# Kernel optimization log

Measured on AMD Instinct MI355X. Metric: run time of the kernel, lower is better.

The kernel has to match this reference:

```python
import jax, jax.numpy as jnp
import numpy as np

N = 50000      # num_nodes
E = 400000     # num_edges
H = 64         # h_dim
R = 200        # num_rels
B = 8          # num_bases (block-diagonal decomposition)


def setup_inputs() -> dict:
    ks = jax.random.split(jax.random.key(0), 10)
    s = 1.0 / np.sqrt(H).astype(np.float32)
    return {
        "emb":     jax.random.normal(ks[0], (N, H), jnp.float32),
        "norm":    jax.random.uniform(ks[1], (E, 1), jnp.float32),
        "eps":     jax.random.normal(ks[2], (N, H), jnp.float32),
        "w1":      jax.random.normal(ks[3], (R, B * 8 * 8), jnp.float32) * s,
        "loop_w1": jax.random.normal(ks[4], (H, H), jnp.float32) * s,
        "b1":      jnp.zeros((H,), jnp.float32),
        "w2":      jax.random.normal(ks[5], (R, B * 8 * 16), jnp.float32) * s,
        "loop_w2": jax.random.normal(ks[6], (H, 2 * H), jnp.float32) * s,
        "b2":      jnp.zeros((2 * H,), jnp.float32),
        "h_ids":   jnp.arange(N, dtype=jnp.int32),
        "src":     jax.random.randint(ks[7], (E,), 0, N, jnp.int32),
        "dst":     jax.random.randint(ks[8], (E,), 0, N, jnp.int32),
        "rel":     jax.random.randint(ks[9], (E,), 0, R, jnp.int32),
    }


def bdd_conv(feat, src, dst, rel, norm, weight, loop_w, bias, out_feat):
    # RelGraphConv with 'bdd' regularizer: per-edge relation-indexed
    # block-diagonal weight gather, bmm message, norm scale, scatter-add,
    # then bias + self-loop.
    n_edges = src.shape[0]
    sub_in = feat.shape[1] // B
    sub_out = out_feat // B
    w = weight[rel].reshape(n_edges, B, sub_in, sub_out)   # gather per edge
    x = feat[src].reshape(n_edges, B, sub_in)
    msg = jnp.einsum('ebi,ebio->ebo', x, w).reshape(n_edges, out_feat) * norm
    agg = jax.ops.segment_sum(msg, dst, num_segments=feat.shape[0])
    return agg + bias + feat @ loop_w


def reference(emb, norm, eps, w1, loop_w1, b1, w2, loop_w2, b2,
              h_ids, src, dst, rel):
    feat = emb[h_ids]                                       # embedding lookup
    h1 = jax.nn.relu(bdd_conv(feat, src, dst, rel, norm, w1, loop_w1, b1, H))
    h2 = bdd_conv(h1, src, dst, rel, norm, w2, loop_w2, b2, 2 * H)
    m, raw_v = jnp.split(h2, 2, axis=-1)                    # gaussian_parameters
    v = jax.nn.softplus(raw_v) + 1e-8
    return m + jnp.sqrt(v) * eps                            # reparameterize
```

## Files before the change

### kernel.cpp

```cpp
#include <hip/hip_runtime.h>
#include <math.h>


typedef __attribute__((ext_vector_type(8))) short bf16x8;
typedef __attribute__((ext_vector_type(4))) float f32x4;
typedef __attribute__((ext_vector_type(2))) float v2f;
typedef __attribute__((ext_vector_type(2))) _Float16 h2;

__device__ __forceinline__ int bcasti(int v, int l) {
    return __builtin_amdgcn_readlane(v, l);
}
__device__ __forceinline__ float bcastf(float v, int l) {
    return __int_as_float(__builtin_amdgcn_readlane(__float_as_int(v), l));
}
__device__ __forceinline__ unsigned short f2bf(float f) {
    unsigned u = __float_as_uint(f);
    return (unsigned short)((u + 0x7FFFu + ((u >> 16) & 1u)) >> 16);
}
__device__ __forceinline__ unsigned short f2h(float f) {
    return __builtin_bit_cast(unsigned short, (_Float16)f);
}
__device__ __forceinline__ float bfs(unsigned short s) { return __uint_as_float((unsigned)s << 16); }
__device__ __forceinline__ h2 uh2(unsigned u) { return __builtin_bit_cast(h2, u); }

__global__ void hist(const int* __restrict__ dst, int* __restrict__ deg, int e) {
    int i = blockIdx.x * blockDim.x + threadIdx.x;
    if (i < e) atomicAdd(&deg[dst[i]], 1);
}

__global__ void scan_part(const int* __restrict__ deg, int* __restrict__ bsum, int n) {
    __shared__ int sm[256];
    int t = threadIdx.x, g = blockIdx.x * 256 + t;
    sm[t] = (g < n) ? deg[g] : 0;
    __syncthreads();
    for (int d = 128; d > 0; d >>= 1) {
        if (t < d) sm[t] += sm[t + d];
        __syncthreads();
    }
    if (t == 0) bsum[blockIdx.x] = sm[0];
}

__global__ void scan_bsum(int* __restrict__ bsum, int* __restrict__ off, int nb, int n) {
    __shared__ int sm[256];
    int t = threadIdx.x;
    int v = (t < nb) ? bsum[t] : 0;
    sm[t] = v;
    __syncthreads();
    for (int d = 1; d < 256; d <<= 1) {
        int u = (t >= d) ? sm[t - d] : 0;
        __syncthreads();
        sm[t] += u;
        __syncthreads();
    }
    if (t < nb) bsum[t] = sm[t] - v;
    if (t == 255) off[n] = sm[255];
}

__global__ void scan_write(const int* __restrict__ deg, const int* __restrict__ bsum,
                           int* __restrict__ off, int n) {
    __shared__ int sm[256];
    int t = threadIdx.x, g = blockIdx.x * 256 + t;
    int v = (g < n) ? deg[g] : 0;
    sm[t] = v;
    __syncthreads();
    for (int d = 1; d < 256; d <<= 1) {
        int u = (t >= d) ? sm[t - d] : 0;
        __syncthreads();
        sm[t] += u;
        __syncthreads();
    }
    if (g < n) off[g] = bsum[blockIdx.x] + sm[t] - v;
}

__global__ void scatter_pack(const int* __restrict__ src, const int* __restrict__ dst,
                             const int* __restrict__ rel, const float* __restrict__ norm,
                             const int* __restrict__ h_ids, const int* __restrict__ off,
                             int* __restrict__ fil, unsigned* __restrict__ packA,
                             unsigned* __restrict__ packB, float* __restrict__ norm_s, int e) {
    int i = blockIdx.x * blockDim.x + threadIdx.x;
    if (i >= e) return;
    int d = dst[i];
    int p = off[d] + atomicAdd(&fil[d], 1);
    unsigned rhi = (unsigned)rel[i] << 16;
    int s = src[i];
    packA[p] = (unsigned)h_ids[s] | rhi;
    packB[p] = (unsigned)s | rhi;
    norm_s[p] = norm[i];
}

__global__ void cvt_all(const float* __restrict__ w1, const float* __restrict__ w2,
                        const float* __restrict__ emb, unsigned short* __restrict__ w1h,
                        unsigned short* __restrict__ w2h, unsigned short* __restrict__ embh,
                        int n1, int n2, int ne) {
    int i = blockIdx.x * blockDim.x + threadIdx.x;
    if (i < n1) w1h[i] = f2h(w1[i]);
    else if (i < n1 + n2) w2h[i - n1] = f2h(w2[i - n1]);
    else if (i < n1 + n2 + ne) embh[i - n1 - n2] = f2bf(emb[i - n1 - n2]);
}

__global__ __launch_bounds__(256) void
gemm1_mfma(const unsigned short* __restrict__ embh, const int* __restrict__ h_ids,
           const float* __restrict__ lw1, const float* __restrict__ b1,
           unsigned short* __restrict__ h1bh, int n_nodes) {
    int w = threadIdx.x >> 6, l = threadIdx.x & 63;
    int lr = l & 15, lq = l >> 4;
    int rt = blockIdx.x;
    bf16x8 bfr[2];
    int coln = w * 16 + lr;
#pragma unroll
    for (int kb = 0; kb < 2; ++kb)
#pragma unroll
        for (int jj = 0; jj < 8; ++jj)
            bfr[kb][jj] = (short)f2bf(lw1[(kb * 32 + lq * 8 + jj) * 64 + coln]);
    int nrow = rt * 16 + lr;
    if (nrow >= n_nodes) nrow = n_nodes - 1;
    const unsigned short* arow = embh + (long)h_ids[nrow] * 64 + lq * 8;
    bf16x8 af0 = *(const bf16x8*)arow;
    bf16x8 af1 = *(const bf16x8*)(arow + 32);
    f32x4 acc = {0.f, 0.f, 0.f, 0.f};
    acc = __builtin_amdgcn_mfma_f32_16x16x32_bf16(af0, bfr[0], acc, 0, 0, 0);
    acc = __builtin_amdgcn_mfma_f32_16x16x32_bf16(af1, bfr[1], acc, 0, 0, 0);
    float bb = b1[coln];
#pragma unroll
    for (int r = 0; r < 4; ++r) {
        int row = rt * 16 + lq * 4 + r;
        if (row < n_nodes) h1bh[(long)row * 64 + coln] = f2bf(acc[r] + bb);
    }
}

__global__ __launch_bounds__(256) void
gemm2_mfma(const unsigned short* __restrict__ h1h, const float* __restrict__ lw2,
           const float* __restrict__ b2, unsigned short* __restrict__ h2bh, int n_nodes) {
    int w = threadIdx.x >> 6, l = threadIdx.x & 63;
    int lr = l & 15, lq = l >> 4;
    int rt = blockIdx.x;
    bf16x8 bfr[2][2];
    int col0 = (2 * w) * 16 + lr, col1 = (2 * w + 1) * 16 + lr;
#pragma unroll
    for (int kb = 0; kb < 2; ++kb)
#pragma unroll
        for (int jj = 0; jj < 8; ++jj) {
            int k = kb * 32 + lq * 8 + jj;
            bfr[0][kb][jj] = (short)f2bf(lw2[k * 128 + col0]);
            bfr[1][kb][jj] = (short)f2bf(lw2[k * 128 + col1]);
        }
    int nrow = rt * 16 + lr;
    if (nrow >= n_nodes) nrow = n_nodes - 1;
    bf16x8 af0 = *(const bf16x8*)(h1h + (long)nrow * 64 + lq * 8);
    bf16x8 af1 = *(const bf16x8*)(h1h + (long)nrow * 64 + 32 + lq * 8);
    f32x4 acc0 = {0.f, 0.f, 0.f, 0.f}, acc1 = {0.f, 0.f, 0.f, 0.f};
    acc0 = __builtin_amdgcn_mfma_f32_16x16x32_bf16(af0, bfr[0][0], acc0, 0, 0, 0);
    acc0 = __builtin_amdgcn_mfma_f32_16x16x32_bf16(af1, bfr[0][1], acc0, 0, 0, 0);
    acc1 = __builtin_amdgcn_mfma_f32_16x16x32_bf16(af0, bfr[1][0], acc1, 0, 0, 0);
    acc1 = __builtin_amdgcn_mfma_f32_16x16x32_bf16(af1, bfr[1][1], acc1, 0, 0, 0);
    float bb0 = b2[col0], bb1 = b2[col1];
#pragma unroll
    for (int r = 0; r < 4; ++r) {
        int row = rt * 16 + lq * 4 + r;
        if (row < n_nodes) {
            h2bh[(long)row * 128 + col0] = f2bf(acc0[r] + bb0);
            h2bh[(long)row * 128 + col1] = f2bf(acc1[r] + bb1);
        }
    }
}

__device__ __forceinline__ float reduce8(float a0, float a1, float a2, float a3,
                                         float a4, float a5, float a6, float a7, int i) {
    int p1 = i & 1, p2 = (i >> 1) & 1, p3 = (i >> 2) & 1;
    float ka, sb, u0, u1, u2, u3, w0, w1;
    ka = p1 ? a1 : a0; sb = p1 ? a0 : a1; u0 = ka + __shfl_xor(sb, 1, 64);
    ka = p1 ? a3 : a2; sb = p1 ? a2 : a3; u1 = ka + __shfl_xor(sb, 1, 64);
    ka = p1 ? a5 : a4; sb = p1 ? a4 : a5; u2 = ka + __shfl_xor(sb, 1, 64);
    ka = p1 ? a7 : a6; sb = p1 ? a6 : a7; u3 = ka + __shfl_xor(sb, 1, 64);
    ka = p2 ? u1 : u0; sb = p2 ? u0 : u1; w0 = ka + __shfl_xor(sb, 2, 64);
    ka = p2 ? u3 : u2; sb = p2 ? u2 : u3; w1 = ka + __shfl_xor(sb, 2, 64);
    ka = p3 ? w1 : w0; sb = p3 ? w0 : w1;
    return ka + __shfl_xor(sb, 4, 64);
}

__global__ __launch_bounds__(256) void
edge1(const unsigned short* __restrict__ embh, const unsigned short* __restrict__ w1h,
      const unsigned short* __restrict__ h1bh, const int* __restrict__ off,
      const unsigned* __restrict__ packA, const float* __restrict__ norm_s,
      unsigned short* __restrict__ h1h, int n_nodes) {
    __shared__ unsigned short xstage[4][8][64];
    int tid = threadIdx.x;
    int w = tid >> 6, j = tid & 63, i = j & 7;
    int cl = j >> 3, il = j & 7;
    int n = blockIdx.x * 4 + w;
    if (n >= n_nodes) return;
    unsigned short* xsw = &xstage[w][0][0];
    float base = bfs(h1bh[(long)n * 64 + j]);
    h2 acc[4];
#pragma unroll
    for (int q = 0; q < 4; ++q) acc[q] = (h2){(_Float16)0.f, (_Float16)0.f};
    int e0 = off[n], e1v = off[n + 1];
    const long woff = (long)j * 8;
    for (int win = e0; win < e1v; win += 64) {
        int wcnt = e1v - win; if (wcnt > 64) wcnt = 64;
        unsigned u = (j < wcnt) ? packA[win + j] : 0u;
        float nmv = (j < wcnt) ? norm_s[win + j] : 0.f;
        for (int b8 = 0; b8 < wcnt; b8 += 8) {
            int cnt = wcnt - b8; if (cnt > 8) cnt = 8;
            int uc = __builtin_amdgcn_ds_bpermute((b8 + cl) << 2, (int)u);
            if (cl < cnt)
                *(bf16x8*)(xsw + (cl << 6) + (il << 3)) =
                    *(const bf16x8*)(embh + (long)((unsigned)uc & 0xFFFFu) * 64 + (il << 3));
            asm volatile("s_waitcnt lgkmcnt(0)" ::: "memory");
#pragma unroll
            for (int c = 0; c < 8; ++c)
                if (c < cnt) {
                    float nm = bcastf(nmv, b8 + c);
                    int rr = bcasti((int)u, b8 + c) >> 16;
                    uint4 wd = *(const uint4*)(w1h + (long)rr * 512 + woff);
                    _Float16 xh = (_Float16)(bfs(xsw[(c << 6) + j]) * nm);
                    h2 xh2 = {xh, xh};
                    acc[0] += xh2 * uh2(wd.x);
                    acc[1] += xh2 * uh2(wd.y);
                    acc[2] += xh2 * uh2(wd.z);
                    acc[3] += xh2 * uh2(wd.w);
                }
        }
    }
    float agg = reduce8((float)acc[0].x, (float)acc[0].y, (float)acc[1].x, (float)acc[1].y,
                        (float)acc[2].x, (float)acc[2].y, (float)acc[3].x, (float)acc[3].y, i);
    h1h[(long)n * 64 + j] = f2bf(fmaxf(base + agg, 0.f));
}

__global__ __launch_bounds__(256) void
edge2(const unsigned short* __restrict__ h1h, const unsigned short* __restrict__ w2h,
      const unsigned short* __restrict__ h2bh, const float* __restrict__ eps,
      const int* __restrict__ off, const unsigned* __restrict__ packB,
      const float* __restrict__ norm_s, float* __restrict__ out, int n_nodes) {
    __shared__ unsigned short xstage[4][8][64];
    int tid = threadIdx.x;
    int w = tid >> 6, j = tid & 63;
    int i = j & 7, b = j >> 3;
    int o1 = b * 16 + i, o2 = o1 + 8;
    int cl = j >> 3, il = j & 7;
    int n = blockIdx.x * 4 + w;
    if (n >= n_nodes) return;
    unsigned short* xsw = &xstage[w][0][0];
    float base1 = bfs(h2bh[(long)n * 128 + o1]);
    float base2 = bfs(h2bh[(long)n * 128 + o2]);
    h2 acc[8];
#pragma unroll
    for (int q = 0; q < 8; ++q) acc[q] = (h2){(_Float16)0.f, (_Float16)0.f};
    int e0 = off[n], e1v = off[n + 1];
    const long woff = (long)j * 16;
    for (int win = e0; win < e1v; win += 64) {
        int wcnt = e1v - win; if (wcnt > 64) wcnt = 64;
        unsigned u = (j < wcnt) ? packB[win + j] : 0u;
        float nmv = (j < wcnt) ? norm_s[win + j] : 0.f;
        for (int b8 = 0; b8 < wcnt; b8 += 8) {
            int cnt = wcnt - b8; if (cnt > 8) cnt = 8;
            int uc = __builtin_amdgcn_ds_bpermute((b8 + cl) << 2, (int)u);
            if (cl < cnt)
                *(bf16x8*)(xsw + (cl << 6) + (il << 3)) =
                    *(const bf16x8*)(h1h + (long)((unsigned)uc & 0xFFFFu) * 64 + (il << 3));
            asm volatile("s_waitcnt lgkmcnt(0)" ::: "memory");
#pragma unroll
            for (int c = 0; c < 8; ++c)
                if (c < cnt) {
                    float nm = bcastf(nmv, b8 + c);
                    int rr = bcasti((int)u, b8 + c) >> 16;
                    const uint4* p = (const uint4*)(w2h + (long)rr * 1024 + woff);
                    uint4 wa = p[0], wb = p[1];
                    _Float16 xh = (_Float16)(bfs(xsw[(c << 6) + j]) * nm);
                    h2 xh2 = {xh, xh};
                    acc[0] += xh2 * uh2(wa.x);
                    acc[1] += xh2 * uh2(wa.y);
                    acc[2] += xh2 * uh2(wa.z);
                    acc[3] += xh2 * uh2(wa.w);
                    acc[4] += xh2 * uh2(wb.x);
                    acc[5] += xh2 * uh2(wb.y);
                    acc[6] += xh2 * uh2(wb.z);
                    acc[7] += xh2 * uh2(wb.w);
                }
        }
    }
    float r1 = reduce8((float)acc[0].x, (float)acc[0].y, (float)acc[1].x, (float)acc[1].y,
                       (float)acc[2].x, (float)acc[2].y, (float)acc[3].x, (float)acc[3].y, i);
    float r2 = reduce8((float)acc[4].x, (float)acc[4].y, (float)acc[5].x, (float)acc[5].y,
                       (float)acc[6].x, (float)acc[6].y, (float)acc[7].x, (float)acc[7].y, i);
    float v1 = r1 + base1;
    float v2 = r2 + base2;
    float p1 = __shfl_xor(v1, 32, 64);
    float p2 = __shfl_xor(v2, 32, 64);
    if (j < 32) {
        long basep = (long)n * 64;
        float sp1 = (p1 > 20.f) ? p1 : log1pf(expf(p1));
        float sp2 = (p2 > 20.f) ? p2 : log1pf(expf(p2));
        out[basep + o1] = fmaf(sqrtf(sp1 + 1e-8f), eps[basep + o1], v1);
        out[basep + o2] = fmaf(sqrtf(sp2 + 1e-8f), eps[basep + o2], v2);
    }
}

extern "C" void kernel_launch(void* const* d_in, const int* in_sizes, int n_in,
                              void* d_out, int out_size, void* d_ws, size_t ws_size,
                              hipStream_t stream) {
    const float* emb   = (const float*)d_in[0];
    const float* norm  = (const float*)d_in[1];
    const float* eps   = (const float*)d_in[2];
    const float* w1    = (const float*)d_in[3];
    const float* lw1   = (const float*)d_in[4];
    const float* b1    = (const float*)d_in[5];
    const float* w2    = (const float*)d_in[6];
    const float* lw2   = (const float*)d_in[7];
    const float* b2    = (const float*)d_in[8];
    const int*   h_ids = (const int*)d_in[9];
    const int*   src   = (const int*)d_in[10];
    const int*   dst   = (const int*)d_in[11];
    const int*   rel   = (const int*)d_in[12];
    float* out = (float*)d_out;

    int n_nodes = in_sizes[0] / 64;
    int n_edges = in_sizes[10];
    int nw1 = in_sizes[3];
    int nw2 = in_sizes[6];
    int ne  = in_sizes[0];

    char* ws = (char*)d_ws;
    unsigned short* h1bh = (unsigned short*)ws;       ws += (size_t)n_nodes * 64 * 2;
    unsigned short* h1h  = (unsigned short*)ws;       ws += (size_t)n_nodes * 64 * 2;
    unsigned short* h2bh = (unsigned short*)ws;       ws += (size_t)n_nodes * 128 * 2;
    unsigned short* embh = (unsigned short*)ws;       ws += (size_t)ne * 2;
    unsigned short* w1h  = (unsigned short*)ws;       ws += (size_t)nw1 * 2;
    unsigned short* w2h  = (unsigned short*)ws;       ws += (size_t)nw2 * 2;
    unsigned* pkA = (unsigned*)ws;                    ws += (size_t)n_edges * 4;
    unsigned* pkB = (unsigned*)ws;                    ws += (size_t)n_edges * 4;
    float* norm_s = (float*)ws;                       ws += (size_t)n_edges * 4;
    int*   deg    = (int*)ws;                         ws += (size_t)n_nodes * 4;
    int*   fil    = (int*)ws;                         ws += (size_t)n_nodes * 4;
    int*   off    = (int*)ws;                         ws += (size_t)(n_nodes + 1) * 4;
    int*   bsum   = (int*)ws;

    int blk = 256;
    int nb = (n_nodes + 255) / 256;
    int nt = (n_nodes + 15) / 16;
    int ng = (n_nodes + 3) / 4;
    hipMemsetAsync(deg, 0, (size_t)n_nodes * 8, stream);
    cvt_all<<<(nw1 + nw2 + ne + blk - 1) / blk, blk, 0, stream>>>(w1, w2, emb, w1h, w2h, embh, nw1, nw2, ne);
    hist<<<(n_edges + blk - 1) / blk, blk, 0, stream>>>(dst, deg, n_edges);
    scan_part<<<nb, 256, 0, stream>>>(deg, bsum, n_nodes);
    scan_bsum<<<1, 256, 0, stream>>>(bsum, off, nb, n_nodes);
    scan_write<<<nb, 256, 0, stream>>>(deg, bsum, off, n_nodes);
    scatter_pack<<<(n_edges + blk - 1) / blk, blk, 0, stream>>>(src, dst, rel, norm, h_ids, off, fil, pkA, pkB, norm_s, n_edges);
    gemm1_mfma<<<nt, blk, 0, stream>>>(embh, h_ids, lw1, b1, h1bh, n_nodes);
    edge1<<<ng, blk, 0, stream>>>(embh, w1h, h1bh, off, pkA, norm_s, h1h, n_nodes);
    gemm2_mfma<<<nt, blk, 0, stream>>>(h1h, lw2, b2, h2bh, n_nodes);
    edge2<<<ng, blk, 0, stream>>>(h1h, w2h, h2bh, eps, off, pkB, norm_s, out, n_nodes);
}
```

Measured before the change: 268.7 us.

## Sort edges by relation and compute messages with per-relation MFMA GEMMs

Adds a relation histogram and scan so edges are bucketed by relation. Each relation's block-diagonal weight is expanded into a dense bf16 64xN matrix and applied to the gathered source features with MFMA. The fp16 messages go to a per-edge buffer, and separate kernels sum them per destination node through a position map. This swaps the per-edge scalar block-diagonal math for tensor-core GEMMs, at the cost of writing and re-reading a large message buffer (E x 128 fp16) and doing 8x redundant FLOPs on the zero blocks. A fallback keeps the old path when the workspace is too small.

```diff
diff --git a/kernel.cpp b/kernel.cpp
--- a/kernel.cpp
+++ b/kernel.cpp
@@ -4,12 +4,9 @@
 
 typedef __attribute__((ext_vector_type(8))) short bf16x8;
 typedef __attribute__((ext_vector_type(4))) float f32x4;
-typedef __attribute__((ext_vector_type(2))) float v2f;
 typedef __attribute__((ext_vector_type(2))) _Float16 h2;
 
-__device__ __forceinline__ int bcasti(int v, int l) {
-    return __builtin_amdgcn_readlane(v, l);
-}
+__device__ __forceinline__ int bcasti(int v, int l) { return __builtin_amdgcn_readlane(v, l); }
 __device__ __forceinline__ float bcastf(float v, int l) {
     return __int_as_float(__builtin_amdgcn_readlane(__float_as_int(v), l));
 }
@@ -17,15 +14,20 @@
     unsigned u = __float_as_uint(f);
     return (unsigned short)((u + 0x7FFFu + ((u >> 16) & 1u)) >> 16);
 }
-__device__ __forceinline__ unsigned short f2h(float f) {
+__device__ __forceinline__ unsigned short f2h16(float f) {
     return __builtin_bit_cast(unsigned short, (_Float16)f);
 }
 __device__ __forceinline__ float bfs(unsigned short s) { return __uint_as_float((unsigned)s << 16); }
 __device__ __forceinline__ h2 uh2(unsigned u) { return __builtin_bit_cast(h2, u); }
 
-__global__ void hist(const int* __restrict__ dst, int* __restrict__ deg, int e) {
+
+__global__ void hist2(const int* __restrict__ dst, const int* __restrict__ rel,
+                      int* __restrict__ deg, int* __restrict__ degr, int e) {
     int i = blockIdx.x * blockDim.x + threadIdx.x;
-    if (i < e) atomicAdd(&deg[dst[i]], 1);
+    if (i < e) {
+        atomicAdd(&deg[dst[i]], 1);
+        atomicAdd(&degr[rel[i]], 1);
+    }
 }
 
 __global__ void scan_part(const int* __restrict__ deg, int* __restrict__ bsum, int n) {
@@ -71,6 +73,301 @@
     }
     if (g < n) off[g] = bsum[blockIdx.x] + sm[t] - v;
 }
+
+__global__ void scan_rel(const int* __restrict__ degr, int* __restrict__ offr, int R) {
+    __shared__ int sm[256];
+    int t = threadIdx.x;
+    int v = (t < R) ? degr[t] : 0;
+    sm[t] = v;
+    __syncthreads();
+    for (int d = 1; d < 256; d <<= 1) {
+        int u = (t >= d) ? sm[t - d] : 0;
+        __syncthreads();
+        sm[t] += u;
+        __syncthreads();
+    }
+    if (t < R) offr[t] = sm[t] - v;
+    if (t == 255) offr[R] = sm[255];
+}
+
+__global__ void scatter2(const int* __restrict__ src, const int* __restrict__ dst,
+                         const int* __restrict__ rel, const float* __restrict__ norm,
+                         const int* __restrict__ h_ids, const int* __restrict__ off,
+                         const int* __restrict__ offr, int* __restrict__ fil,
+                         int* __restrict__ filr, int* __restrict__ pos,
+                         int* __restrict__ xidA, int* __restrict__ xidB,
+                         float* __restrict__ nrm, int e) {
+    int i = blockIdx.x * blockDim.x + threadIdx.x;
+    if (i >= e) return;
+    int d = dst[i], r = rel[i], s = src[i];
+    int p = offr[r] + atomicAdd(&filr[r], 1);
+    int q = off[d] + atomicAdd(&fil[d], 1);
+    pos[q] = p;
+    xidA[p] = h_ids[s];
+    xidB[p] = s;
+    nrm[p] = norm[i];
+}
+
+
+__global__ void cvt_new(const float* __restrict__ w1, const float* __restrict__ w2,
+                        const float* __restrict__ emb, unsigned short* __restrict__ w1dT,
+                        unsigned short* __restrict__ w2dT, unsigned short* __restrict__ embh,
+                        int R, int ne) {
+    int i = blockIdx.x * blockDim.x + threadIdx.x;
+    int n1d = R * 4096, n2d = R * 8192;
+    if (i < n1d) {
+        int r = i >> 12, rem = i & 4095;
+        int c = rem >> 6, k = rem & 63;
+        int b = k >> 3;
+        float v = (b == (c >> 3)) ? w1[(size_t)r * 512 + b * 64 + (k & 7) * 8 + (c & 7)] : 0.f;
+        w1dT[i] = f2bf(v);
+    } else if (i < n1d + n2d) {
+        int ii = i - n1d;
+        int r = ii >> 13, rem = ii & 8191;
+        int c = rem >> 6, k = rem & 63;
+        int b = k >> 3;
+        float v = (b == (c >> 4)) ? w2[(size_t)r * 1024 + b * 128 + (k & 7) * 16 + (c & 15)] : 0.f;
+        w2dT[ii] = f2bf(v);
+    } else if (i < n1d + n2d + ne) {
+        int ii = i - n1d - n2d;
+        embh[ii] = f2bf(emb[ii]);
+    }
+}
+
+__global__ void cvt_old(const float* __restrict__ w1, const float* __restrict__ w2,
+                        const float* __restrict__ emb, unsigned short* __restrict__ w1h,
+                        unsigned short* __restrict__ w2h, unsigned short* __restrict__ embh,
+                        int n1, int n2, int ne) {
+    int i = blockIdx.x * blockDim.x + threadIdx.x;
+    if (i < n1) w1h[i] = f2h16(w1[i]);
+    else if (i < n1 + n2) w2h[i - n1] = f2h16(w2[i - n1]);
+    else if (i < n1 + n2 + ne) embh[i - n1 - n2] = f2bf(emb[i - n1 - n2]);
+}
+
+
+__global__ __launch_bounds__(256) void
+gemm1_mfma(const unsigned short* __restrict__ embh, const int* __restrict__ h_ids,
+           const float* __restrict__ lw1, const float* __restrict__ b1,
+           unsigned short* __restrict__ h1bh, int n_nodes) {
+    int w = threadIdx.x >> 6, l = threadIdx.x & 63;
+    int lr = l & 15, lq = l >> 4;
+    int rt = blockIdx.x;
+    bf16x8 bfr[2];
+    int coln = w * 16 + lr;
+#pragma unroll
+    for (int kb = 0; kb < 2; ++kb)
+#pragma unroll
+        for (int jj = 0; jj < 8; ++jj)
+            bfr[kb][jj] = (short)f2bf(lw1[(kb * 32 + lq * 8 + jj) * 64 + coln]);
+    int nrow = rt * 16 + lr;
+    if (nrow >= n_nodes) nrow = n_nodes - 1;
+    const unsigned short* arow = embh + (long)h_ids[nrow] * 64 + lq * 8;
+    bf16x8 af0 = *(const bf16x8*)arow;
+    bf16x8 af1 = *(const bf16x8*)(arow + 32);
+    f32x4 acc = {0.f, 0.f, 0.f, 0.f};
+    acc = __builtin_amdgcn_mfma_f32_16x16x32_bf16(af0, bfr[0], acc, 0, 0, 0);
+    acc = __builtin_amdgcn_mfma_f32_16x16x32_bf16(af1, bfr[1], acc, 0, 0, 0);
+    float bb = b1[coln];
+#pragma unroll
+    for (int r = 0; r < 4; ++r) {
+        int row = rt * 16 + lq * 4 + r;
+        if (row < n_nodes) h1bh[(long)row * 64 + coln] = f2bf(acc[r] + bb);
+    }
+}
+
+__global__ __launch_bounds__(256) void
+gemm2_mfma(const unsigned short* __restrict__ h1h, const float* __restrict__ lw2,
+           const float* __restrict__ b2, unsigned short* __restrict__ h2bh, int n_nodes) {
+    int w = threadIdx.x >> 6, l = threadIdx.x & 63;
+    int lr = l & 15, lq = l >> 4;
+    int rt = blockIdx.x;
+    bf16x8 bfr[2][2];
+    int col0 = (2 * w) * 16 + lr, col1 = (2 * w + 1) * 16 + lr;
+#pragma unroll
+    for (int kb = 0; kb < 2; ++kb)
+#pragma unroll
+        for (int jj = 0; jj < 8; ++jj) {
+            int k = kb * 32 + lq * 8 + jj;
+            bfr[0][kb][jj] = (short)f2bf(lw2[k * 128 + col0]);
+            bfr[1][kb][jj] = (short)f2bf(lw2[k * 128 + col1]);
+        }
+    int nrow = rt * 16 + lr;
+    if (nrow >= n_nodes) nrow = n_nodes - 1;
+    bf16x8 af0 = *(const bf16x8*)(h1h + (long)nrow * 64 + lq * 8);
+    bf16x8 af1 = *(const bf16x8*)(h1h + (long)nrow * 64 + 32 + lq * 8);
+    f32x4 acc0 = {0.f, 0.f, 0.f, 0.f}, acc1 = {0.f, 0.f, 0.f, 0.f};
+    acc0 = __builtin_amdgcn_mfma_f32_16x16x32_bf16(af0, bfr[0][0], acc0, 0, 0, 0);
+    acc0 = __builtin_amdgcn_mfma_f32_16x16x32_bf16(af1, bfr[0][1], acc0, 0, 0, 0);
+    acc1 = __builtin_amdgcn_mfma_f32_16x16x32_bf16(af0, bfr[1][0], acc1, 0, 0, 0);
+    acc1 = __builtin_amdgcn_mfma_f32_16x16x32_bf16(af1, bfr[1][1], acc1, 0, 0, 0);
+    float bb0 = b2[col0], bb1 = b2[col1];
+#pragma unroll
+    for (int r = 0; r < 4; ++r) {
+        int row = rt * 16 + lq * 4 + r;
+        if (row < n_nodes) {
+            h2bh[(long)row * 128 + col0] = f2bf(acc0[r] + bb0);
+            h2bh[(long)row * 128 + col1] = f2bf(acc1[r] + bb1);
+        }
+    }
+}
+
+
+__global__ __launch_bounds__(256) void
+gemm_rel1(const unsigned short* __restrict__ embh, const unsigned short* __restrict__ w1dT,
+          const int* __restrict__ xidA, const float* __restrict__ nrm,
+          const int* __restrict__ offr, _Float16* __restrict__ msg1, int S) {
+    int r = blockIdx.x / S, s = blockIdx.x % S;
+    int w = threadIdx.x >> 6, l = threadIdx.x & 63;
+    int lr = l & 15, lq = l >> 4;
+    int e0r = offr[r], e1r = offr[r + 1];
+    if (e0r >= e1r) return;
+    bf16x8 bfr[4][2];
+    const unsigned short* wb = w1dT + (size_t)r * 4096;
+#pragma unroll
+    for (int ct = 0; ct < 4; ++ct)
+#pragma unroll
+        for (int kb = 0; kb < 2; ++kb)
+            bfr[ct][kb] = *(const bf16x8*)(wb + (ct * 16 + lr) * 64 + kb * 32 + lq * 8);
+    for (int t = s * 4 + w;; t += S * 4) {
+        int t16 = e0r + t * 16;
+        if (t16 >= e1r) break;
+        int erow = t16 + lr;
+        int erc = erow < e1r ? erow : e1r - 1;
+        const unsigned short* arow = embh + (size_t)xidA[erc] * 64 + lq * 8;
+        bf16x8 af0 = *(const bf16x8*)arow;
+        bf16x8 af1 = *(const bf16x8*)(arow + 32);
+        f32x4 acc[4];
+#pragma unroll
+        for (int ct = 0; ct < 4; ++ct) {
+            acc[ct] = (f32x4){0.f, 0.f, 0.f, 0.f};
+            acc[ct] = __builtin_amdgcn_mfma_f32_16x16x32_bf16(af0, bfr[ct][0], acc[ct], 0, 0, 0);
+            acc[ct] = __builtin_amdgcn_mfma_f32_16x16x32_bf16(af1, bfr[ct][1], acc[ct], 0, 0, 0);
+        }
+#pragma unroll
+        for (int r4 = 0; r4 < 4; ++r4) {
+            int orow = t16 + lq * 4 + r4;
+            int orc = orow < e1r ? orow : e1r - 1;
+            float nm = nrm[orc];
+            if (orow < e1r) {
+#pragma unroll
+                for (int ct = 0; ct < 4; ++ct)
+                    msg1[(size_t)orow * 64 + ct * 16 + lr] = (_Float16)(acc[ct][r4] * nm);
+            }
+        }
+    }
+}
+
+__global__ __launch_bounds__(256) void
+gemm_rel2(const unsigned short* __restrict__ h1h, const unsigned short* __restrict__ w2dT,
+          const int* __restrict__ xidB, const float* __restrict__ nrm,
+          const int* __restrict__ offr, _Float16* __restrict__ msg2, int S) {
+    int r = blockIdx.x / S, s = blockIdx.x % S;
+    int w = threadIdx.x >> 6, l = threadIdx.x & 63;
+    int lr = l & 15, lq = l >> 4;
+    int e0r = offr[r], e1r = offr[r + 1];
+    if (e0r >= e1r) return;
+    bf16x8 bfr[8][2];
+    const unsigned short* wb = w2dT + (size_t)r * 8192;
+#pragma unroll
+    for (int ct = 0; ct < 8; ++ct)
+#pragma unroll
+        for (int kb = 0; kb < 2; ++kb)
+            bfr[ct][kb] = *(const bf16x8*)(wb + (ct * 16 + lr) * 64 + kb * 32 + lq * 8);
+    for (int t = s * 4 + w;; t += S * 4) {
+        int t16 = e0r + t * 16;
+        if (t16 >= e1r) break;
+        int erow = t16 + lr;
+        int erc = erow < e1r ? erow : e1r - 1;
+        const unsigned short* arow = h1h + (size_t)xidB[erc] * 64 + lq * 8;
+        bf16x8 af0 = *(const bf16x8*)arow;
+        bf16x8 af1 = *(const bf16x8*)(arow + 32);
+        f32x4 acc[8];
+#pragma unroll
+        for (int ct = 0; ct < 8; ++ct) {
+            acc[ct] = (f32x4){0.f, 0.f, 0.f, 0.f};
+            acc[ct] = __builtin_amdgcn_mfma_f32_16x16x32_bf16(af0, bfr[ct][0], acc[ct], 0, 0, 0);
+            acc[ct] = __builtin_amdgcn_mfma_f32_16x16x32_bf16(af1, bfr[ct][1], acc[ct], 0, 0, 0);
+        }
+#pragma unroll
+        for (int r4 = 0; r4 < 4; ++r4) {
+            int orow = t16 + lq * 4 + r4;
+            int orc = orow < e1r ? orow : e1r - 1;
+            float nm = nrm[orc];
+            if (orow < e1r) {
+#pragma unroll
+                for (int ct = 0; ct < 8; ++ct)
+                    msg2[(size_t)orow * 128 + ct * 16 + lr] = (_Float16)(acc[ct][r4] * nm);
+            }
+        }
+    }
+}
+
+
+__global__ __launch_bounds__(256) void
+sum1(const _Float16* __restrict__ msg1, const int* __restrict__ pos,
+     const unsigned short* __restrict__ h1bh, const int* __restrict__ off,
+     unsigned short* __restrict__ h1h, int n_nodes) {
+    int tid = threadIdx.x;
+    int w = tid >> 6, j = tid & 63;
+    int n = blockIdx.x * 4 + w;
+    if (n >= n_nodes) return;
+    float base = bfs(h1bh[(size_t)n * 64 + j]);
+    int e0 = off[n], e1v = off[n + 1];
+    float a0 = 0.f, a1 = 0.f, a2 = 0.f, a3 = 0.f;
+    for (int win = e0; win < e1v; win += 64) {
+        int wcnt = e1v - win; if (wcnt > 64) wcnt = 64;
+        int pv = (j < wcnt) ? pos[win + j] : 0;
+        int c = 0;
+        for (; c + 4 <= wcnt; c += 4) {
+            int p0 = bcasti(pv, c), p1 = bcasti(pv, c + 1);
+            int p2 = bcasti(pv, c + 2), p3 = bcasti(pv, c + 3);
+            a0 += (float)msg1[(size_t)p0 * 64 + j];
+            a1 += (float)msg1[(size_t)p1 * 64 + j];
+            a2 += (float)msg1[(size_t)p2 * 64 + j];
+            a3 += (float)msg1[(size_t)p3 * 64 + j];
+        }
+        for (; c < wcnt; ++c)
+            a0 += (float)msg1[(size_t)bcasti(pv, c) * 64 + j];
+    }
+    float s = a0 + a1 + a2 + a3 + base;
+    h1h[(size_t)n * 64 + j] = f2bf(fmaxf(s, 0.f));
+}
+
+__global__ __launch_bounds__(256) void
+sum2(const _Float16* __restrict__ msg2, const int* __restrict__ pos,
+     const unsigned short* __restrict__ h2bh, const float* __restrict__ eps,
+     const int* __restrict__ off, float* __restrict__ out, int n_nodes) {
+    int tid = threadIdx.x;
+    int w = tid >> 6, j = tid & 63;
+    int n = blockIdx.x * 4 + w;
+    if (n >= n_nodes) return;
+    float basem = bfs(h2bh[(size_t)n * 128 + j]);
+    float basev = bfs(h2bh[(size_t)n * 128 + 64 + j]);
+    int e0 = off[n], e1v = off[n + 1];
+    float m0 = 0.f, m1 = 0.f, v0 = 0.f, v1a = 0.f;
+    for (int win = e0; win < e1v; win += 64) {
+        int wcnt = e1v - win; if (wcnt > 64) wcnt = 64;
+        int pv = (j < wcnt) ? pos[win + j] : 0;
+        int c = 0;
+        for (; c + 2 <= wcnt; c += 2) {
+            int p0 = bcasti(pv, c), p1 = bcasti(pv, c + 1);
+            m0 += (float)msg2[(size_t)p0 * 128 + j];
+            v0 += (float)msg2[(size_t)p0 * 128 + 64 + j];
+            m1 += (float)msg2[(size_t)p1 * 128 + j];
+            v1a += (float)msg2[(size_t)p1 * 128 + 64 + j];
+        }
+        for (; c < wcnt; ++c) {
+            int p0 = bcasti(pv, c);
+            m0 += (float)msg2[(size_t)p0 * 128 + j];
+            v0 += (float)msg2[(size_t)p0 * 128 + 64 + j];
+        }
+    }
+    float vm = m0 + m1 + basem;
+    float vv = v0 + v1a + basev;
+    float sp = (vv > 20.f) ? vv : log1pf(expf(vv));
+    out[(size_t)n * 64 + j] = fmaf(sqrtf(sp + 1e-8f), eps[(size_t)n * 64 + j], vm);
+}
+
 
 __global__ void scatter_pack(const int* __restrict__ src, const int* __restrict__ dst,
                              const int* __restrict__ rel, const float* __restrict__ norm,
@@ -86,82 +383,6 @@
     packA[p] = (unsigned)h_ids[s] | rhi;
     packB[p] = (unsigned)s | rhi;
     norm_s[p] = norm[i];
-}
-
-__global__ void cvt_all(const float* __restrict__ w1, const float* __restrict__ w2,
-                        const float* __restrict__ emb, unsigned short* __restrict__ w1h,
-                        unsigned short* __restrict__ w2h, unsigned short* __restrict__ embh,
-                        int n1, int n2, int ne) {
-    int i = blockIdx.x * blockDim.x + threadIdx.x;
-    if (i < n1) w1h[i] = f2h(w1[i]);
-    else if (i < n1 + n2) w2h[i - n1] = f2h(w2[i - n1]);
-    else if (i < n1 + n2 + ne) embh[i - n1 - n2] = f2bf(emb[i - n1 - n2]);
-}
-
-__global__ __launch_bounds__(256) void
-gemm1_mfma(const unsigned short* __restrict__ embh, const int* __restrict__ h_ids,
-           const float* __restrict__ lw1, const float* __restrict__ b1,
-           unsigned short* __restrict__ h1bh, int n_nodes) {
-    int w = threadIdx.x >> 6, l = threadIdx.x & 63;
-    int lr = l & 15, lq = l >> 4;
-    int rt = blockIdx.x;
-    bf16x8 bfr[2];
-    int coln = w * 16 + lr;
-#pragma unroll
-    for (int kb = 0; kb < 2; ++kb)
-#pragma unroll
-        for (int jj = 0; jj < 8; ++jj)
-            bfr[kb][jj] = (short)f2bf(lw1[(kb * 32 + lq * 8 + jj) * 64 + coln]);
-    int nrow = rt * 16 + lr;
-    if (nrow >= n_nodes) nrow = n_nodes - 1;
-    const unsigned short* arow = embh + (long)h_ids[nrow] * 64 + lq * 8;
-    bf16x8 af0 = *(const bf16x8*)arow;
-    bf16x8 af1 = *(const bf16x8*)(arow + 32);
-    f32x4 acc = {0.f, 0.f, 0.f, 0.f};
-    acc = __builtin_amdgcn_mfma_f32_16x16x32_bf16(af0, bfr[0], acc, 0, 0, 0);
-    acc = __builtin_amdgcn_mfma_f32_16x16x32_bf16(af1, bfr[1], acc, 0, 0, 0);
-    float bb = b1[coln];
-#pragma unroll
-    for (int r = 0; r < 4; ++r) {
-        int row = rt * 16 + lq * 4 + r;
-        if (row < n_nodes) h1bh[(long)row * 64 + coln] = f2bf(acc[r] + bb);
-    }
-}
-
-__global__ __launch_bounds__(256) void
-gemm2_mfma(const unsigned short* __restrict__ h1h, const float* __restrict__ lw2,
-           const float* __restrict__ b2, unsigned short* __restrict__ h2bh, int n_nodes) {
-    int w = threadIdx.x >> 6, l = threadIdx.x & 63;
-    int lr = l & 15, lq = l >> 4;
-    int rt = blockIdx.x;
-    bf16x8 bfr[2][2];
-    int col0 = (2 * w) * 16 + lr, col1 = (2 * w + 1) * 16 + lr;
-#pragma unroll
-    for (int kb = 0; kb < 2; ++kb)
-#pragma unroll
-        for (int jj = 0; jj < 8; ++jj) {
-            int k = kb * 32 + lq * 8 + jj;
-            bfr[0][kb][jj] = (short)f2bf(lw2[k * 128 + col0]);
-            bfr[1][kb][jj] = (short)f2bf(lw2[k * 128 + col1]);
-        }
-    int nrow = rt * 16 + lr;
-    if (nrow >= n_nodes) nrow = n_nodes - 1;
-    bf16x8 af0 = *(const bf16x8*)(h1h + (long)nrow * 64 + lq * 8);
-    bf16x8 af1 = *(const bf16x8*)(h1h + (long)nrow * 64 + 32 + lq * 8);
-    f32x4 acc0 = {0.f, 0.f, 0.f, 0.f}, acc1 = {0.f, 0.f, 0.f, 0.f};
-    acc0 = __builtin_amdgcn_mfma_f32_16x16x32_bf16(af0, bfr[0][0], acc0, 0, 0, 0);
-    acc0 = __builtin_amdgcn_mfma_f32_16x16x32_bf16(af1, bfr[0][1], acc0, 0, 0, 0);
-    acc1 = __builtin_amdgcn_mfma_f32_16x16x32_bf16(af0, bfr[1][0], acc1, 0, 0, 0);
-    acc1 = __builtin_amdgcn_mfma_f32_16x16x32_bf16(af1, bfr[1][1], acc1, 0, 0, 0);
-    float bb0 = b2[col0], bb1 = b2[col1];
-#pragma unroll
-    for (int r = 0; r < 4; ++r) {
-        int row = rt * 16 + lq * 4 + r;
-        if (row < n_nodes) {
-            h2bh[(long)row * 128 + col0] = f2bf(acc0[r] + bb0);
-            h2bh[(long)row * 128 + col1] = f2bf(acc1[r] + bb1);
-        }
-    }
 }
 
 __device__ __forceinline__ float reduce8(float a0, float a1, float a2, float a3,
@@ -296,6 +517,7 @@
     }
 }
 
+
 extern "C" void kernel_launch(void* const* d_in, const int* in_sizes, int n_in,
                               void* d_out, int out_size, void* d_ws, size_t ws_size,
                               hipStream_t stream) {
@@ -319,35 +541,92 @@
     int nw1 = in_sizes[3];
     int nw2 = in_sizes[6];
     int ne  = in_sizes[0];
-
-    char* ws = (char*)d_ws;
-    unsigned short* h1bh = (unsigned short*)ws;       ws += (size_t)n_nodes * 64 * 2;
-    unsigned short* h1h  = (unsigned short*)ws;       ws += (size_t)n_nodes * 64 * 2;
-    unsigned short* h2bh = (unsigned short*)ws;       ws += (size_t)n_nodes * 128 * 2;
-    unsigned short* embh = (unsigned short*)ws;       ws += (size_t)ne * 2;
-    unsigned short* w1h  = (unsigned short*)ws;       ws += (size_t)nw1 * 2;
-    unsigned short* w2h  = (unsigned short*)ws;       ws += (size_t)nw2 * 2;
-    unsigned* pkA = (unsigned*)ws;                    ws += (size_t)n_edges * 4;
-    unsigned* pkB = (unsigned*)ws;                    ws += (size_t)n_edges * 4;
-    float* norm_s = (float*)ws;                       ws += (size_t)n_edges * 4;
-    int*   deg    = (int*)ws;                         ws += (size_t)n_nodes * 4;
-    int*   fil    = (int*)ws;                         ws += (size_t)n_nodes * 4;
-    int*   off    = (int*)ws;                         ws += (size_t)(n_nodes + 1) * 4;
-    int*   bsum   = (int*)ws;
+    int R   = nw1 / 512;
 
     int blk = 256;
     int nb = (n_nodes + 255) / 256;
     int nt = (n_nodes + 15) / 16;
     int ng = (n_nodes + 3) / 4;
-    hipMemsetAsync(deg, 0, (size_t)n_nodes * 8, stream);
-    cvt_all<<<(nw1 + nw2 + ne + blk - 1) / blk, blk, 0, stream>>>(w1, w2, emb, w1h, w2h, embh, nw1, nw2, ne);
-    hist<<<(n_edges + blk - 1) / blk, blk, 0, stream>>>(dst, deg, n_edges);
-    scan_part<<<nb, 256, 0, stream>>>(deg, bsum, n_nodes);
-    scan_bsum<<<1, 256, 0, stream>>>(bsum, off, nb, n_nodes);
-    scan_write<<<nb, 256, 0, stream>>>(deg, bsum, off, n_nodes);
-    scatter_pack<<<(n_edges + blk - 1) / blk, blk, 0, stream>>>(src, dst, rel, norm, h_ids, off, fil, pkA, pkB, norm_s, n_edges);
-    gemm1_mfma<<<nt, blk, 0, stream>>>(embh, h_ids, lw1, b1, h1bh, n_nodes);
-    edge1<<<ng, blk, 0, stream>>>(embh, w1h, h1bh, off, pkA, norm_s, h1h, n_nodes);
-    gemm2_mfma<<<nt, blk, 0, stream>>>(h1h, lw2, b2, h2bh, n_nodes);
-    edge2<<<ng, blk, 0, stream>>>(h1h, w2h, h2bh, eps, off, pkB, norm_s, out, n_nodes);
-}
+
+    size_t need = (size_t)ne * 2
+                + (size_t)n_nodes * 64 * 2 * 2
+                + (size_t)n_nodes * 128 * 2
+                + (size_t)R * 4096 * 2
+                + (size_t)R * 8192 * 2
+                + (size_t)n_edges * 4 * 4
+                + (size_t)n_edges * 128 * 2
+                + (size_t)(2 * n_nodes + 2 * R) * 4
+                + (size_t)(n_nodes + 1) * 4
+                + (size_t)(R + 1) * 4
+                + (size_t)nb * 4;
+
+    if (ws_size >= need) {
+        char* p = (char*)d_ws;
+        unsigned short* embh = (unsigned short*)p;  p += (size_t)ne * 2;
+        unsigned short* h1bh = (unsigned short*)p;  p += (size_t)n_nodes * 64 * 2;
+        unsigned short* h1h  = (unsigned short*)p;  p += (size_t)n_nodes * 64 * 2;
+        unsigned short* h2bh = (unsigned short*)p;  p += (size_t)n_nodes * 128 * 2;
+        unsigned short* w1dT = (unsigned short*)p;  p += (size_t)R * 4096 * 2;
+        unsigned short* w2dT = (unsigned short*)p;  p += (size_t)R * 8192 * 2;
+        int*   xidA = (int*)p;                      p += (size_t)n_edges * 4;
+        int*   xidB = (int*)p;                      p += (size_t)n_edges * 4;
+        float* nrm  = (float*)p;                    p += (size_t)n_edges * 4;
+        int*   pos  = (int*)p;                      p += (size_t)n_edges * 4;
+        _Float16* msg = (_Float16*)p;               p += (size_t)n_edges * 128 * 2;
+        int* deg  = (int*)p;                        p += (size_t)n_nodes * 4;
+        int* fil  = (int*)p;                        p += (size_t)n_nodes * 4;
+        int* degr = (int*)p;                        p += (size_t)R * 4;
+        int* filr = (int*)p;                        p += (size_t)R * 4;
+        int* off  = (int*)p;                        p += (size_t)(n_nodes + 1) * 4;
+        int* offr = (int*)p;                        p += (size_t)(R + 1) * 4;
+        int* bsum = (int*)p;
+
+        const int S = 8;
+        int ncv = R * 4096 + R * 8192 + ne;
+        hipMemsetAsync(deg, 0, (size_t)(2 * n_nodes + 2 * R) * 4, stream);
+        cvt_new<<<(ncv + blk - 1) / blk, blk, 0, stream>>>(w1, w2, emb, w1dT, w2dT, embh, R, ne);
+        hist2<<<(n_edges + blk - 1) / blk, blk, 0, stream>>>(dst, rel, deg, degr, n_edges);
+        scan_part<<<nb, 256, 0, stream>>>(deg, bsum, n_nodes);
+        scan_bsum<<<1, 256, 0, stream>>>(bsum, off, nb, n_nodes);
+        scan_write<<<nb, 256, 0, stream>>>(deg, bsum, off, n_nodes);
+        scan_rel<<<1, 256, 0, stream>>>(degr, offr, R);
+        scatter2<<<(n_edges + blk - 1) / blk, blk, 0, stream>>>(
+            src, dst, rel, norm, h_ids, off, offr, fil, filr, pos, xidA, xidB, nrm, n_edges);
+        gemm1_mfma<<<nt, blk, 0, stream>>>(embh, h_ids, lw1, b1, h1bh, n_nodes);
+        gemm_rel1<<<R * S, blk, 0, stream>>>(embh, w1dT, xidA, nrm, offr, msg, S);
+        sum1<<<ng, blk, 0, stream>>>(msg, pos, h1bh, off, h1h, n_nodes);
+        gemm2_mfma<<<nt, blk, 0, stream>>>(h1h, lw2, b2, h2bh, n_nodes);
+        gemm_rel2<<<R * S, blk, 0, stream>>>(h1h, w2dT, xidB, nrm, offr, msg, S);
+        sum2<<<ng, blk, 0, stream>>>(msg, pos, h2bh, eps, off, out, n_nodes);
+    } else {
+        char* p = (char*)d_ws;
+        unsigned short* h1bh = (unsigned short*)p;  p += (size_t)n_nodes * 64 * 2;
+        unsigned short* h1h  = (unsigned short*)p;  p += (size_t)n_nodes * 64 * 2;
+        unsigned short* h2bh = (unsigned short*)p;  p += (size_t)n_nodes * 128 * 2;
+        unsigned short* embh = (unsigned short*)p;  p += (size_t)ne * 2;
+        unsigned short* w1h  = (unsigned short*)p;  p += (size_t)nw1 * 2;
+        unsigned short* w2h  = (unsigned short*)p;  p += (size_t)nw2 * 2;
+        unsigned* pkA = (unsigned*)p;               p += (size_t)n_edges * 4;
+        unsigned* pkB = (unsigned*)p;               p += (size_t)n_edges * 4;
+        float* norm_s = (float*)p;                  p += (size_t)n_edges * 4;
+        int* deg  = (int*)p;                        p += (size_t)n_nodes * 4;
+        int* fil  = (int*)p;                        p += (size_t)n_nodes * 4;
+        int* degr = (int*)p;                        p += (size_t)R * 4;
+        int* filr = (int*)p;                        p += (size_t)R * 4;
+        int* off  = (int*)p;                        p += (size_t)(n_nodes + 1) * 4;
+        int* bsum = (int*)p;
+
+        hipMemsetAsync(deg, 0, (size_t)(2 * n_nodes + 2 * R) * 4, stream);
+        cvt_old<<<(nw1 + nw2 + ne + blk - 1) / blk, blk, 0, stream>>>(w1, w2, emb, w1h, w2h, embh, nw1, nw2, ne);
+        hist2<<<(n_edges + blk - 1) / blk, blk, 0, stream>>>(dst, rel, deg, degr, n_edges);
+        scan_part<<<nb, 256, 0, stream>>>(deg, bsum, n_nodes);
+        scan_bsum<<<1, 256, 0, stream>>>(bsum, off, nb, n_nodes);
+        scan_write<<<nb, 256, 0, stream>>>(deg, bsum, off, n_nodes);
+        scatter_pack<<<(n_edges + blk - 1) / blk, blk, 0, stream>>>(
+            src, dst, rel, norm, h_ids, off, fil, pkA, pkB, norm_s, n_edges);
+        gemm1_mfma<<<nt, blk, 0, stream>>>(embh, h_ids, lw1, b1, h1bh, n_nodes);
+        edge1<<<ng, blk, 0, stream>>>(embh, w1h, h1bh, off, pkA, norm_s, h1h, n_nodes);
+        gemm2_mfma<<<nt, blk, 0, stream>>>(h1h, lw2, b2, h2bh, n_nodes);
+        edge2<<<ng, blk, 0, stream>>>(h1h, w2h, h2bh, eps, off, pkB, norm_s, out, n_nodes);
+    }
+}
```

After: 731.0 us. 172% more time.
